# Kernel tuning notes

Hardware: AMD Instinct MI355X
Metric: run time of the kernel (lower is better)

The kernel has to match this reference:

```python
import jax, jax.numpy as jnp
import numpy as np

B, C, E = 4, 2048, 1024
H, D = 16, 64


def setup_inputs() -> dict:
    key = jax.random.key(0)
    kx, kq, kk, kv, ko = jax.random.split(key, 5)
    s = 0.02
    return {
        "x": jax.random.normal(kx, (B, C, E), dtype=jnp.float32),
        "W_q": jax.random.normal(kq, (E, H * D), dtype=jnp.float32) * s,
        "W_k": jax.random.normal(kk, (E, H * D), dtype=jnp.float32) * s,
        "W_v": jax.random.normal(kv, (E, H * D), dtype=jnp.float32) * s,
        "W_o": jax.random.normal(ko, (H * D, E), dtype=jnp.float32) * s,
    }


def reference(x, W_q, W_k, W_v, W_o):
    b, c, e = x.shape
    # projections -> [B, H, C, D]
    def split_heads(t):
        return t.reshape(b, c, H, D).transpose(0, 2, 1, 3)
    Q = split_heads(x @ W_q)
    K = split_heads(x @ W_k)
    V = split_heads(x @ W_v)
    scale = 1.0 / jnp.sqrt(jnp.asarray(D, dtype=x.dtype))
    scores = jnp.einsum("bhqd,bhkd->bhqk", Q, K) * scale  # [B,H,C,C]
    causal = jnp.tril(jnp.ones((c, c), dtype=bool))
    scores = jnp.where(causal, scores, jnp.asarray(-jnp.inf, dtype=scores.dtype))
    weights = jax.nn.softmax(scores, axis=-1)
    hidden = jnp.einsum("bhqk,bhkd->bhqd", weights, V)  # [B,H,C,D]
    hidden = hidden.transpose(0, 2, 1, 3).reshape(b, c, H * D)
    return hidden @ W_o
```

## Files before the change

kernel.cpp:

```cpp
#include <hip/hip_runtime.h>

typedef __bf16 bf16;
typedef __attribute__((ext_vector_type(8))) __bf16 bf16x8;
typedef __attribute__((ext_vector_type(4))) __bf16 bf16x4;
typedef __attribute__((ext_vector_type(4))) float f32x4;
typedef __attribute__((ext_vector_type(16))) float f32x16;

#define B_ 4
#define C_ 2048
#define E_ 1024
#define H_ 16
#define D_ 64

__device__ __forceinline__ void gload16(const void* g, void* l) {
  __builtin_amdgcn_global_load_lds(
      (const __attribute__((address_space(1))) void*)g,
      (__attribute__((address_space(3))) void*)l, 16, 0, 0);
}

__device__ __forceinline__ unsigned cvtpk(float lo, float hi) {
  unsigned r;
  asm("v_cvt_pk_bf16_f32 %0, %1, %2" : "=v"(r) : "v"(lo), "v"(hi));
  return r;
}
__device__ __forceinline__ void pswap(unsigned& a, unsigned& b) {
  asm volatile("v_permlane32_swap_b32 %0, %1" : "+v"(a), "+v"(b));
}
__device__ __forceinline__ bf16x8 mkfrag(unsigned d0, unsigned d1, unsigned d2,
                                         unsigned d3) {
  union {
    unsigned u[4];
    bf16x8 v;
  } x;
  x.u[0] = d0;
  x.u[1] = d1;
  x.u[2] = d2;
  x.u[3] = d3;
  return x.v;
}

__global__ __launch_bounds__(256) void prep(const float* __restrict__ x,
                                            const float* __restrict__ Wq,
                                            const float* __restrict__ Wk,
                                            const float* __restrict__ Wv,
                                            const float* __restrict__ Wo,
                                            bf16* __restrict__ xb,
                                            bf16* __restrict__ WT) {
  if (blockIdx.z < 4) {
    const float* W = blockIdx.z == 0 ? Wq : blockIdx.z == 1 ? Wk
                   : blockIdx.z == 2 ? Wv : Wo;
    bf16* dst = WT + (size_t)blockIdx.z * 1024 * 1024;
    __shared__ bf16 t[64][65];
    const int tx = threadIdx.x & 63, ty = threadIdx.x >> 6;
    const int r0 = blockIdx.y * 64, c0 = blockIdx.x * 64;
#pragma unroll
    for (int r = ty; r < 64; r += 4)
      t[tx][r] = (__bf16)W[(size_t)(r0 + r) * 1024 + c0 + tx];
    __syncthreads();
#pragma unroll
    for (int r = ty; r < 64; r += 4)
      dst[(size_t)(c0 + r) * 1024 + r0 + tx] = t[r][tx];
  } else {
    const size_t chunk =
        ((size_t)(blockIdx.z - 4) * 256 + blockIdx.y * 16 + blockIdx.x);
    const size_t i = chunk * 256 + threadIdx.x;
    const float4* p = (const float4*)(x + i * 8);
    float4 a = p[0], b = p[1];
    bf16x8 v = {(__bf16)a.x, (__bf16)a.y, (__bf16)a.z, (__bf16)a.w,
                (__bf16)b.x, (__bf16)b.y, (__bf16)b.z, (__bf16)b.w};
    *(bf16x8*)(xb + i * 8) = v;
  }
}

template <int MODE>
__global__ __launch_bounds__(256, 2) void gemm_bt(const bf16* __restrict__ A,
                                                  const bf16* __restrict__ WTall,
                                                  bf16* __restrict__ Qo,
                                                  bf16* __restrict__ Ko,
                                                  bf16* __restrict__ Vto,
                                                  float* __restrict__ Fo) {
  constexpr int BK = 64;
  constexpr int NT = 1024 / BK;
  const int tid = threadIdx.x;
  const int wave = tid >> 6, lane = tid & 63;
  const int cl = lane & 15, g = lane >> 4;
  const int wr = wave >> 1, wc = wave & 1;
  const int brow = blockIdx.x * 128;
  const int bcol = blockIdx.y * 128;
  const bf16* Bt =
      (MODE == 0) ? (WTall + (size_t)blockIdx.z * 1024 * 1024) : WTall;

  __shared__ __align__(16) bf16 ldsA[2][128 * BK];
  __shared__ __align__(16) bf16 ldsB[2][128 * BK];

  f32x4 acc[4][4] = {};

  auto STAGE = [&](int kt, int buf) {
#pragma unroll
    for (int it = 0; it < 4; ++it) {
      const int chunk = it * 256 + tid;
      const int row = chunk >> 3, slot = chunk & 7;
      const int se = (slot ^ (row & 7)) * 8;
      const int ldsoff = (it * 256 + wave * 64) * 16;
      gload16(A + (size_t)(brow + row) * 1024 + kt + se,
              (char*)&ldsA[buf][0] + ldsoff);
      gload16(Bt + (size_t)(bcol + row) * 1024 + kt + se,
              (char*)&ldsB[buf][0] + ldsoff);
    }
  };

  STAGE(0, 0);
  STAGE(BK, 1);
  asm volatile("s_waitcnt vmcnt(8)" ::: "memory");
  __builtin_amdgcn_s_barrier();

  for (int t = 0; t < NT; ++t) {
    const int buf = t & 1;
    bf16x8 af[2][4], bfr[2][4];
#pragma unroll
    for (int kkid = 0; kkid < 2; ++kkid) {
#pragma unroll
      for (int i = 0; i < 4; ++i) {
        const int sl = ((4 * kkid + g) ^ (cl & 7)) * 8;
        af[kkid][i] = *(const bf16x8*)&ldsA[buf][(wr * 64 + i * 16 + cl) * BK + sl];
        bfr[kkid][i] = *(const bf16x8*)&ldsB[buf][(wc * 64 + i * 16 + cl) * BK + sl];
      }
    }
    asm volatile("s_waitcnt lgkmcnt(0)" ::: "memory");
    __builtin_amdgcn_sched_barrier(0);
    __builtin_amdgcn_s_barrier();

    if (t + 2 < NT) STAGE((t + 2) * BK, buf);

#pragma unroll
    for (int kkid = 0; kkid < 2; ++kkid)
#pragma unroll
      for (int i = 0; i < 4; ++i)
#pragma unroll
        for (int j = 0; j < 4; ++j)
          acc[i][j] = __builtin_amdgcn_mfma_f32_16x16x32_bf16(
              af[kkid][i], bfr[kkid][j], acc[i][j], 0, 0, 0);

    if (t + 2 < NT)
      asm volatile("s_waitcnt vmcnt(8)" ::: "memory");
    else
      asm volatile("s_waitcnt vmcnt(0)" ::: "memory");
    __builtin_amdgcn_s_barrier();
  }

  bf16* dst = nullptr;
  if constexpr (MODE == 0)
    dst = blockIdx.z == 0 ? Qo : blockIdx.z == 1 ? Ko : Vto;
  const float presc =
      (MODE == 0 && blockIdx.z == 0) ? 0.18033688011112042f : 1.0f;
#pragma unroll
  for (int i = 0; i < 4; ++i) {
#pragma unroll
    for (int j = 0; j < 4; ++j) {
#pragma unroll
      for (int r = 0; r < 4; ++r) {
        const int gr = brow + wr * 64 + i * 16 + g * 4 + r;
        const int gc = bcol + wc * 64 + j * 16 + cl;
        const float v = acc[i][j][r] * presc;
        if constexpr (MODE == 0) {
          const int b = gr >> 11, c = gr & 2047;
          const int h = gc >> 6, d = gc & 63;
          if (blockIdx.z == 2)
            dst[(((size_t)b * H_ + h) * D_ + d) * C_ + c] = (__bf16)v;
          else
            dst[(((size_t)b * H_ + h) * C_ + c) * D_ + d] = (__bf16)v;
        } else {
          Fo[(size_t)gr * 1024 + gc] = v;
        }
      }
    }
  }
}

__device__ __forceinline__ void sm_fixed(f32x16& s0, f32x16& s1, f32x4& l4,
                                         int th0, bool domask, int hi,
                                         bf16x8& pf0, bf16x8& pf1,
                                         bf16x8& pf2, bf16x8& pf3) {
  if (domask) {
#pragma unroll
    for (int r = 0; r < 16; ++r) {
      const int crow = (r & 3) + 8 * (r >> 2) + 4 * hi;
      if (crow > th0) s0[r] = -1e30f;
      if (crow + 32 > th0) s1[r] = -1e30f;
    }
  }
#pragma unroll
  for (int r = 0; r < 16; ++r) {
    s0[r] = __builtin_amdgcn_exp2f(s0[r]);
    s1[r] = __builtin_amdgcn_exp2f(s1[r]);
  }
#pragma unroll
  for (int r = 0; r < 16; ++r) l4[r & 3] += s0[r] + s1[r];
  unsigned a0 = cvtpk(s0[0], s0[1]), a1 = cvtpk(s0[2], s0[3]);
  unsigned b0 = cvtpk(s0[4], s0[5]), b1 = cvtpk(s0[6], s0[7]);
  unsigned c0 = cvtpk(s0[8], s0[9]), c1 = cvtpk(s0[10], s0[11]);
  unsigned d0 = cvtpk(s0[12], s0[13]), d1 = cvtpk(s0[14], s0[15]);
  unsigned e0 = cvtpk(s1[0], s1[1]), e1 = cvtpk(s1[2], s1[3]);
  unsigned f0 = cvtpk(s1[4], s1[5]), f1 = cvtpk(s1[6], s1[7]);
  unsigned g0 = cvtpk(s1[8], s1[9]), g1 = cvtpk(s1[10], s1[11]);
  unsigned h0 = cvtpk(s1[12], s1[13]), h1 = cvtpk(s1[14], s1[15]);
  pswap(a0, b0);
  pswap(a1, b1);
  pswap(c0, d0);
  pswap(c1, d1);
  pswap(e0, f0);
  pswap(e1, f1);
  pswap(g0, h0);
  pswap(g1, h1);
  pf0 = mkfrag(a0, a1, b0, b1);
  pf1 = mkfrag(c0, c1, d0, d1);
  pf2 = mkfrag(e0, e1, f0, f1);
  pf3 = mkfrag(g0, g1, h0, h1);
}

__global__ __launch_bounds__(256, 2) void attn(const bf16* __restrict__ Qg,
                                               const bf16* __restrict__ Kg,
                                               const bf16* __restrict__ Vt,
                                               bf16* __restrict__ Hid) {
  const int tid = threadIdx.x, wave = tid >> 6, lane = tid & 63;
  const int l31 = lane & 31, hi = lane >> 5, l7 = lane & 7;
  const int qa = blockIdx.x, qb = 15 - (int)blockIdx.x;
  const int h = blockIdx.y, b = blockIdx.z;
  const size_t bh = (size_t)b * H_ + h;

  __shared__ __align__(16) bf16 ldsK[2 * 128 * 64];
  __shared__ __align__(16) bf16 ldsV[2 * 64 * 128];

  const bf16* Kb = Kg + bh * C_ * D_;
  const bf16* Vb = Vt + bh * (size_t)D_ * C_;

  const int qrowA = qa * 128 + wave * 32;
  const int qrowB = qb * 128 + wave * 32;

  bf16x8 qfA[4], qfB[4];
  {
    const bf16* qra = Qg + (bh * C_ + qrowA + l31) * D_;
    const bf16* qrb = Qg + (bh * C_ + qrowB + l31) * D_;
#pragma unroll
    for (int ds = 0; ds < 4; ++ds) {
      qfA[ds] = *(const bf16x8*)(qra + ds * 16 + 8 * hi);
      qfB[ds] = *(const bf16x8*)(qrb + ds * 16 + 8 * hi);
    }
  }

  f32x4 l4A = {}, l4B = {};
  f32x16 oA0 = {}, oA1 = {}, oB0 = {}, oB1 = {};

  auto STAGE = [&](int kt, int buf) {
#pragma unroll
    for (int w = 0; w < 4; ++w) {
      const int chunk = w * 256 + tid;
      {
        const int row = chunk >> 3, slot = chunk & 7;
        const int se = (slot ^ (row & 7)) * 8;
        gload16(Kb + ((size_t)kt * 128 + row) * D_ + se,
                (char*)ldsK + buf * 16384 + (w * 256 + wave * 64) * 16);
      }
      {
        const int row = chunk >> 4, slot = chunk & 15;
        const int se = (slot ^ (row & 7)) * 8;
        gload16(Vb + (size_t)row * C_ + kt * 128 + se,
                (char*)ldsV + buf * 16384 + (w * 256 + wave * 64) * 16);
      }
    }
  };

  const int nkv = qb + 1;
  STAGE(0, 0);

  for (int kt = 0; kt < nkv; ++kt) {
    const int cur = kt & 1;
    const bf16* kb = ldsK + cur * 8192;
    const bf16* vb = ldsV + cur * 8192;
    if (kt + 1 < nkv) {
      STAGE(kt + 1, cur ^ 1);
      asm volatile("s_waitcnt vmcnt(8)" ::: "memory");
    } else {
      asm volatile("s_waitcnt vmcnt(0)" ::: "memory");
    }
    __builtin_amdgcn_s_barrier();
    __builtin_amdgcn_sched_barrier(0);

#pragma unroll
    for (int hh = 0; hh < 2; ++hh) {
      const int key0 = kt * 128 + hh * 64;
      const bool actA = (key0 <= qrowA + 31);
      const bool actB = (key0 <= qrowB + 31);
      if (!actA && !actB) continue;

      f32x16 sA0 = {}, sA1 = {}, sB0 = {}, sB1 = {};
      __builtin_amdgcn_s_setprio(1);
#pragma unroll
      for (int ds = 0; ds < 4; ++ds) {
        const int r0 = hh * 64 + l31, r1 = hh * 64 + 32 + l31;
        bf16x8 kf0 = *(const bf16x8*)&kb[r0 * 64 + (((2 * ds + hi) ^ (r0 & 7)) * 8)];
        bf16x8 kf1 = *(const bf16x8*)&kb[r1 * 64 + (((2 * ds + hi) ^ (r1 & 7)) * 8)];
        if (actA) {
          sA0 = __builtin_amdgcn_mfma_f32_32x32x16_bf16(kf0, qfA[ds], sA0, 0, 0, 0);
          sA1 = __builtin_amdgcn_mfma_f32_32x32x16_bf16(kf1, qfA[ds], sA1, 0, 0, 0);
        }
        if (actB) {
          sB0 = __builtin_amdgcn_mfma_f32_32x32x16_bf16(kf0, qfB[ds], sB0, 0, 0, 0);
          sB1 = __builtin_amdgcn_mfma_f32_32x32x16_bf16(kf1, qfB[ds], sB1, 0, 0, 0);
        }
      }
      __builtin_amdgcn_s_setprio(0);

      bf16x8 vf0[4], vf1[4];
#pragma unroll
      for (int ks = 0; ks < 4; ++ks) {
        const int gs = hh * 8 + 2 * ks + hi;
        vf0[ks] = *(const bf16x8*)&vb[l31 * 128 + ((gs ^ (l31 & 7)) * 8)];
        vf1[ks] = *(const bf16x8*)&vb[(32 + l31) * 128 + ((gs ^ ((32 + l31) & 7)) * 8)];
      }

      if (actA) {
        bf16x8 p0, p1, p2, p3;
        sm_fixed(sA0, sA1, l4A, qrowA + l31 - key0, key0 + 63 > qrowA, hi,
                 p0, p1, p2, p3);
        __builtin_amdgcn_s_setprio(1);
        oA0 = __builtin_amdgcn_mfma_f32_32x32x16_bf16(vf0[0], p0, oA0, 0, 0, 0);
        oA1 = __builtin_amdgcn_mfma_f32_32x32x16_bf16(vf1[0], p0, oA1, 0, 0, 0);
        oA0 = __builtin_amdgcn_mfma_f32_32x32x16_bf16(vf0[1], p1, oA0, 0, 0, 0);
        oA1 = __builtin_amdgcn_mfma_f32_32x32x16_bf16(vf1[1], p1, oA1, 0, 0, 0);
        oA0 = __builtin_amdgcn_mfma_f32_32x32x16_bf16(vf0[2], p2, oA0, 0, 0, 0);
        oA1 = __builtin_amdgcn_mfma_f32_32x32x16_bf16(vf1[2], p2, oA1, 0, 0, 0);
        oA0 = __builtin_amdgcn_mfma_f32_32x32x16_bf16(vf0[3], p3, oA0, 0, 0, 0);
        oA1 = __builtin_amdgcn_mfma_f32_32x32x16_bf16(vf1[3], p3, oA1, 0, 0, 0);
        __builtin_amdgcn_s_setprio(0);
      }
      if (actB) {
        bf16x8 p0, p1, p2, p3;
        sm_fixed(sB0, sB1, l4B, qrowB + l31 - key0, key0 + 63 > qrowB, hi,
                 p0, p1, p2, p3);
        __builtin_amdgcn_s_setprio(1);
        oB0 = __builtin_amdgcn_mfma_f32_32x32x16_bf16(vf0[0], p0, oB0, 0, 0, 0);
        oB1 = __builtin_amdgcn_mfma_f32_32x32x16_bf16(vf1[0], p0, oB1, 0, 0, 0);
        oB0 = __builtin_amdgcn_mfma_f32_32x32x16_bf16(vf0[1], p1, oB0, 0, 0, 0);
        oB1 = __builtin_amdgcn_mfma_f32_32x32x16_bf16(vf1[1], p1, oB1, 0, 0, 0);
        oB0 = __builtin_amdgcn_mfma_f32_32x32x16_bf16(vf0[2], p2, oB0, 0, 0, 0);
        oB1 = __builtin_amdgcn_mfma_f32_32x32x16_bf16(vf1[2], p2, oB1, 0, 0, 0);
        oB0 = __builtin_amdgcn_mfma_f32_32x32x16_bf16(vf0[3], p3, oB0, 0, 0, 0);
        oB1 = __builtin_amdgcn_mfma_f32_32x32x16_bf16(vf1[3], p3, oB1, 0, 0, 0);
        __builtin_amdgcn_s_setprio(0);
      }
    }
    __builtin_amdgcn_s_barrier();
  }

#pragma unroll
  for (int st = 0; st < 2; ++st) {
    const f32x4 l4 = st ? l4B : l4A;
    float l = (l4[0] + l4[1]) + (l4[2] + l4[3]);
    l += __shfl_xor(l, 32, 64);
    const float inv = 1.0f / l;
    const int qrow = st ? qrowB : qrowA;
    const size_t row = (size_t)b * C_ + qrow + l31;
#pragma unroll
    for (int dt = 0; dt < 2; ++dt) {
      const f32x16& oo = st ? (dt ? oB1 : oB0) : (dt ? oA1 : oA0);
#pragma unroll
      for (int q4 = 0; q4 < 4; ++q4) {
        bf16x4 pk = {(__bf16)(oo[4 * q4 + 0] * inv),
                     (__bf16)(oo[4 * q4 + 1] * inv),
                     (__bf16)(oo[4 * q4 + 2] * inv),
                     (__bf16)(oo[4 * q4 + 3] * inv)};
        const int d = dt * 32 + 8 * q4 + 4 * hi;
        *(bf16x4*)&Hid[row * (H_ * D_) + h * 64 + d] = pk;
      }
    }
  }
}

extern "C" void kernel_launch(void* const* d_in, const int* in_sizes, int n_in,
                              void* d_out, int out_size, void* d_ws,
                              size_t ws_size, hipStream_t stream) {
  const float* x = (const float*)d_in[0];
  const float* Wq = (const float*)d_in[1];
  const float* Wk = (const float*)d_in[2];
  const float* Wv = (const float*)d_in[3];
  const float* Wo = (const float*)d_in[4];

  char* ws = (char*)d_ws;
  bf16* xb = (bf16*)ws;
  bf16* WT = (bf16*)(ws + (16ull << 20));
  bf16* Qb = (bf16*)(ws + (24ull << 20));
  bf16* Kb = (bf16*)(ws + (40ull << 20));
  bf16* Vtb = (bf16*)(ws + (56ull << 20));
  bf16* Hid = (bf16*)(ws + (72ull << 20));

  prep<<<dim3(16, 16, 20), 256, 0, stream>>>(x, Wq, Wk, Wv, Wo, xb, WT);
  gemm_bt<0><<<dim3(64, 8, 3), 256, 0, stream>>>(xb, WT, Qb, Kb, Vtb, nullptr);
  attn<<<dim3(8, H_, B_), 256, 0, stream>>>(Qb, Kb, Vtb, Hid);
  gemm_bt<1><<<dim3(64, 8, 1), 256, 0, stream>>>(
      Hid, WT + 3ull * 1024 * 1024, nullptr, nullptr, nullptr, (float*)d_out);
}
```

Baseline: 157.5 us.

## Split LDS fragment loads to overlap with MFMA; stage V transpose through LDS

The GEMM main loop now loads the two k-halves of its fragments separately and waits with lgkmcnt(8), so the first batch of MFMAs can start while the second half is still arriving from LDS. The global prefetch of stage t+2 now runs after all MFMAs rather than between the barrier and the compute. For the V projection, the transposed output is written into LDS first and then stored as contiguous 16-byte vectors, instead of scattered 2-byte stores with a stride of C. The risks are less overlap between global prefetch and compute, and extra syncs plus reuse of the ldsA buffer in the epilogue.

Result: faster. 153.7 us (-2.4%).

```diff
diff --git a/kernel.cpp b/kernel.cpp
--- a/kernel.cpp
+++ b/kernel.cpp
@@ -116,64 +116,103 @@
 
   for (int t = 0; t < NT; ++t) {
     const int buf = t & 1;
-    bf16x8 af[2][4], bfr[2][4];
-#pragma unroll
-    for (int kkid = 0; kkid < 2; ++kkid) {
-#pragma unroll
-      for (int i = 0; i < 4; ++i) {
-        const int sl = ((4 * kkid + g) ^ (cl & 7)) * 8;
-        af[kkid][i] = *(const bf16x8*)&ldsA[buf][(wr * 64 + i * 16 + cl) * BK + sl];
-        bfr[kkid][i] = *(const bf16x8*)&ldsB[buf][(wc * 64 + i * 16 + cl) * BK + sl];
-      }
-    }
+    bf16x8 af0[4], bf0[4], af1[4], bf1[4];
+#pragma unroll
+    for (int i = 0; i < 4; ++i) {
+      const int sl = (g ^ (cl & 7)) * 8;
+      af0[i] = *(const bf16x8*)&ldsA[buf][(wr * 64 + i * 16 + cl) * BK + sl];
+      bf0[i] = *(const bf16x8*)&ldsB[buf][(wc * 64 + i * 16 + cl) * BK + sl];
+    }
+    __builtin_amdgcn_sched_barrier(0);
+#pragma unroll
+    for (int i = 0; i < 4; ++i) {
+      const int sl = ((4 + g) ^ (cl & 7)) * 8;
+      af1[i] = *(const bf16x8*)&ldsA[buf][(wr * 64 + i * 16 + cl) * BK + sl];
+      bf1[i] = *(const bf16x8*)&ldsB[buf][(wc * 64 + i * 16 + cl) * BK + sl];
+    }
+    asm volatile("s_waitcnt lgkmcnt(8)" ::: "memory");
+    __builtin_amdgcn_sched_barrier(0);
+#pragma unroll
+    for (int i = 0; i < 4; ++i)
+#pragma unroll
+      for (int j = 0; j < 4; ++j)
+        acc[i][j] = __builtin_amdgcn_mfma_f32_16x16x32_bf16(af0[i], bf0[j],
+                                                            acc[i][j], 0, 0, 0);
     asm volatile("s_waitcnt lgkmcnt(0)" ::: "memory");
     __builtin_amdgcn_sched_barrier(0);
+#pragma unroll
+    for (int i = 0; i < 4; ++i)
+#pragma unroll
+      for (int j = 0; j < 4; ++j)
+        acc[i][j] = __builtin_amdgcn_mfma_f32_16x16x32_bf16(af1[i], bf1[j],
+                                                            acc[i][j], 0, 0, 0);
     __builtin_amdgcn_s_barrier();
-
-    if (t + 2 < NT) STAGE((t + 2) * BK, buf);
-
-#pragma unroll
-    for (int kkid = 0; kkid < 2; ++kkid)
-#pragma unroll
-      for (int i = 0; i < 4; ++i)
-#pragma unroll
-        for (int j = 0; j < 4; ++j)
-          acc[i][j] = __builtin_amdgcn_mfma_f32_16x16x32_bf16(
-              af[kkid][i], bfr[kkid][j], acc[i][j], 0, 0, 0);
-
-    if (t + 2 < NT)
+    if (t + 2 < NT) {
+      STAGE((t + 2) * BK, buf);
       asm volatile("s_waitcnt vmcnt(8)" ::: "memory");
-    else
+    } else {
       asm volatile("s_waitcnt vmcnt(0)" ::: "memory");
+    }
     __builtin_amdgcn_s_barrier();
   }
 
-  bf16* dst = nullptr;
-  if constexpr (MODE == 0)
-    dst = blockIdx.z == 0 ? Qo : blockIdx.z == 1 ? Ko : Vto;
-  const float presc =
-      (MODE == 0 && blockIdx.z == 0) ? 0.18033688011112042f : 1.0f;
-#pragma unroll
-  for (int i = 0; i < 4; ++i) {
-#pragma unroll
-    for (int j = 0; j < 4; ++j) {
-#pragma unroll
-      for (int r = 0; r < 4; ++r) {
-        const int gr = brow + wr * 64 + i * 16 + g * 4 + r;
-        const int gc = bcol + wc * 64 + j * 16 + cl;
-        const float v = acc[i][j][r] * presc;
-        if constexpr (MODE == 0) {
-          const int b = gr >> 11, c = gr & 2047;
-          const int h = gc >> 6, d = gc & 63;
-          if (blockIdx.z == 2)
-            dst[(((size_t)b * H_ + h) * D_ + d) * C_ + c] = (__bf16)v;
-          else
+  if constexpr (MODE == 0) {
+    if (blockIdx.z == 2) {
+      bf16* tb = &ldsA[0][0];
+#pragma unroll
+      for (int i = 0; i < 4; ++i) {
+#pragma unroll
+        for (int j = 0; j < 4; ++j) {
+          const int gc_l = wc * 64 + j * 16 + cl;
+          const int gr0 = wr * 64 + i * 16 + g * 4;
+          bf16x4 pk = {(__bf16)acc[i][j][0], (__bf16)acc[i][j][1],
+                       (__bf16)acc[i][j][2], (__bf16)acc[i][j][3]};
+          *(bf16x4*)&tb[gc_l * 128 + (gr0 ^ ((gc_l & 7) << 4))] = pk;
+        }
+      }
+      __syncthreads();
+      const int b = brow >> 11;
+      const int cbase = brow & 2047;
+#pragma unroll
+      for (int p = 0; p < 8; ++p) {
+        const int rowl = p * 16 + (tid >> 4);
+        const int col0 = (tid & 15) * 8;
+        bf16x8 vv = *(const bf16x8*)&tb[rowl * 128 + (col0 ^ ((rowl & 7) << 4))];
+        const int gc = bcol + rowl;
+        const int hh = gc >> 6, dd = gc & 63;
+        *(bf16x8*)&Vto[(((size_t)b * H_ + hh) * D_ + dd) * C_ + cbase + col0] =
+            vv;
+      }
+    } else {
+      bf16* dst = blockIdx.z == 0 ? Qo : Ko;
+      const float presc = (blockIdx.z == 0) ? 0.18033688011112042f : 1.0f;
+#pragma unroll
+      for (int i = 0; i < 4; ++i) {
+#pragma unroll
+        for (int j = 0; j < 4; ++j) {
+#pragma unroll
+          for (int r = 0; r < 4; ++r) {
+            const int gr = brow + wr * 64 + i * 16 + g * 4 + r;
+            const int gc = bcol + wc * 64 + j * 16 + cl;
+            const float v = acc[i][j][r] * presc;
+            const int b = gr >> 11, c = gr & 2047;
+            const int h = gc >> 6, d = gc & 63;
             dst[(((size_t)b * H_ + h) * C_ + c) * D_ + d] = (__bf16)v;
-        } else {
-          Fo[(size_t)gr * 1024 + gc] = v;
+          }
         }
       }
     }
+  } else {
+#pragma unroll
+    for (int i = 0; i < 4; ++i)
+#pragma unroll
+      for (int j = 0; j < 4; ++j)
+#pragma unroll
+        for (int r = 0; r < 4; ++r) {
+          const int gr = brow + wr * 64 + i * 16 + g * 4 + r;
+          const int gc = bcol + wc * 64 + j * 16 + cl;
+          Fo[(size_t)gr * 1024 + gc] = acc[i][j][r];
+        }
   }
 }
 
```
